# Kernel tuning notes

Hardware: AMD Instinct MI355X
Metric: run time of the kernel (lower is better)

The kernel has to match this reference:

```python
import jax, jax.numpy as jnp
import numpy as np

BATCH, IN_DIM, OUT_DIM = 4096, 8192, 16384

# Each of the 16 logic gates is affine in {1, a, b, a*b}. Rows below give the
# coefficients (const, a, b, ab) for gate k, matching the torch `gate` match-case.
_GATE_COEFS = np.array([
    [0, 0, 0, 0],    # 0: zeros
    [0, 0, 0, 1],    # 1: a*b
    [0, 1, 0, -1],   # 2: a - a*b
    [0, 1, 0, 0],    # 3: a
    [0, 0, 1, -1],   # 4: b - a*b
    [0, 0, 1, 0],    # 5: b
    [0, 1, 1, -2],   # 6: a + b - 2ab (xor)
    [0, 1, 1, -1],   # 7: a + b - ab (or)
    [1, -1, -1, 1],  # 8: 1 - (a + b - ab) (nor)
    [1, -1, -1, 2],  # 9: 1 - (a + b - 2ab) (xnor)
    [1, 0, -1, 0],   # 10: 1 - b
    [1, 0, -1, 1],   # 11: 1 - b + ab
    [1, -1, 0, 0],   # 12: 1 - a
    [1, -1, 0, 1],   # 13: 1 - a + ab
    [1, 0, 0, -1],   # 14: 1 - ab (nand)
    [1, 0, 0, 0],    # 15: ones
], dtype=np.float32)


def setup_inputs() -> dict:
    key = jax.random.key(0)
    k1, k2, k3, k4 = jax.random.split(key, 4)
    x = jax.random.uniform(k1, (BATCH, IN_DIM), dtype=jnp.float32)
    weights = jax.random.normal(k2, (OUT_DIM, 16), dtype=jnp.float32)
    idx_a = jax.random.randint(k3, (OUT_DIM,), 0, IN_DIM, dtype=jnp.int32)
    idx_b = jax.random.randint(k4, (OUT_DIM,), 0, IN_DIM, dtype=jnp.int32)
    return {"x": x, "weights": weights, "idx_a": idx_a, "idx_b": idx_b}


def reference(x, weights, idx_a, idx_b):
    # Training path: softmax over the 16 gate logits per output neuron.
    w = jax.nn.softmax(weights, axis=-1)            # [O, 16]
    # Collapse the 16-gate weighted sum into 4 affine coefficients per neuron.
    coef = w @ jnp.asarray(_GATE_COEFS)             # [O, 4] -> (c0, ca, cb, cab)
    a = x[..., idx_a]                               # [B, O] gather
    b = x[..., idx_b]                               # [B, O] gather
    return coef[:, 0] + coef[:, 1] * a + coef[:, 2] * b + coef[:, 3] * (a * b)
```

## Files before the change

kernel.cpp:

```cpp
#include <hip/hip_runtime.h>
#include <cstddef>
#include <cstdint>

constexpr int BATCH   = 4096;
constexpr int IN_DIM  = 8192;
constexpr int OUT_DIM = 16384;
constexpr int THREADS = 512;
constexpr int RPB     = 4;
constexpr int NBLK    = BATCH / RPB;
constexpr int OPT     = 4;
constexpr int CHUNKS  = OUT_DIM / (THREADS * OPT);
constexpr int SSTEPS  = (IN_DIM / 4) / THREADS;

typedef float    f32x4 __attribute__((ext_vector_type(4)));
typedef uint32_t u32x2 __attribute__((ext_vector_type(2)));

__device__ __forceinline__ uint32_t f2bf(float f) {
  uint32_t u = __float_as_uint(f);
  u += 0x7fffu + ((u >> 16) & 1u);
  return u >> 16;
}
__device__ __forceinline__ uint32_t pack_bf(float a, float b) {
  return f2bf(a) | (f2bf(b) << 16);
}
__device__ __forceinline__ float bf_lo(uint32_t u) { return __uint_as_float(u << 16); }
__device__ __forceinline__ float bf_hi(uint32_t u) { return __uint_as_float(u & 0xffff0000u); }

__global__ __launch_bounds__(64)
void coef_kernel(const float* __restrict__ weights,
                 const int* __restrict__ idx_a,
                 const int* __restrict__ idx_b,
                 float4* __restrict__ coef,
                 uint32_t* __restrict__ pidx) {
  const int o = blockIdx.x * 64 + threadIdx.x;
  if (o >= OUT_DIM) return;

  const float4* wp = reinterpret_cast<const float4*>(weights + (size_t)o * 16);
  float4 t0 = wp[0], t1 = wp[1], t2 = wp[2], t3 = wp[3];
  float w[16] = { t0.x, t0.y, t0.z, t0.w, t1.x, t1.y, t1.z, t1.w,
                  t2.x, t2.y, t2.z, t2.w, t3.x, t3.y, t3.z, t3.w };
  float m = w[0];
#pragma unroll
  for (int i = 1; i < 16; ++i) m = fmaxf(m, w[i]);
  float p[16]; float s = 0.f;
#pragma unroll
  for (int i = 0; i < 16; ++i) { p[i] = __expf(w[i] - m); s += p[i]; }
  const float inv = 1.0f / s;
  const float GC[16]  = {0,0,0,0, 0,0,0,0, 1,1,1,1, 1,1,1,1};
  const float GA[16]  = {0,0,1,1, 0,0,1,1, -1,-1,0,0, -1,-1,0,0};
  const float GB[16]  = {0,0,0,0, 1,1,1,1, -1,-1,-1,-1, 0,0,0,0};
  const float GAB[16] = {0,1,-1,0, -1,0,-2,-1, 1,2,0,1, 0,1,-1,0};
  float c0 = 0.f, ca = 0.f, cb = 0.f, cab = 0.f;
#pragma unroll
  for (int i = 0; i < 16; ++i) {
    c0 += p[i] * GC[i]; ca += p[i] * GA[i];
    cb += p[i] * GB[i]; cab += p[i] * GAB[i];
  }
  coef[o] = make_float4(c0 * inv, ca * inv, cb * inv, cab * inv);
  pidx[o] = (uint32_t)idx_a[o] | ((uint32_t)idx_b[o] << 16);
}

__device__ __forceinline__ float2 eval2(float4 c, uint32_t ga, uint32_t gb) {
  const float a0 = bf_lo(ga), b0 = bf_lo(gb);
  const float a1 = bf_hi(ga), b1 = bf_hi(gb);
  float2 r;
  r.x = fmaf(fmaf(c.w, a0, c.z), b0, fmaf(c.y, a0, c.x));
  r.y = fmaf(fmaf(c.w, a1, c.z), b1, fmaf(c.y, a1, c.x));
  return r;
}

__global__ __launch_bounds__(THREADS)
void logic_main(const float* __restrict__ x,
                const float4* __restrict__ coef,
                const uint32_t* __restrict__ pidx,
                float* __restrict__ out) {
  __shared__ u32x2 xq[IN_DIM];

  const int t  = threadIdx.x;
  const int b0 = blockIdx.x * RPB;

  const f32x4* __restrict__ r0 =
      reinterpret_cast<const f32x4*>(x + (size_t)(b0 + 0) * IN_DIM);
  const f32x4* __restrict__ r1 =
      reinterpret_cast<const f32x4*>(x + (size_t)(b0 + 1) * IN_DIM);
  const f32x4* __restrict__ r2 =
      reinterpret_cast<const f32x4*>(x + (size_t)(b0 + 2) * IN_DIM);
  const f32x4* __restrict__ r3 =
      reinterpret_cast<const f32x4*>(x + (size_t)(b0 + 3) * IN_DIM);

  int o0 = t * OPT;
  int4   pi = *reinterpret_cast<const int4*>(pidx + o0);
  float4 c0 = coef[o0 + 0], c1 = coef[o0 + 1],
         c2 = coef[o0 + 2], c3 = coef[o0 + 3];

#pragma unroll
  for (int s = 0; s < SSTEPS; ++s) {
    const int q = s * THREADS + t;
    f32x4 a = r0[q], b = r1[q], c = r2[q], d = r3[q];
    u32x2 p0, p1, p2, p3;
    p0.x = pack_bf(a.x, b.x); p0.y = pack_bf(c.x, d.x);
    p1.x = pack_bf(a.y, b.y); p1.y = pack_bf(c.y, d.y);
    p2.x = pack_bf(a.z, b.z); p2.y = pack_bf(c.z, d.z);
    p3.x = pack_bf(a.w, b.w); p3.y = pack_bf(c.w, d.w);
    xq[4 * q + 0] = p0;
    xq[4 * q + 1] = p1;
    xq[4 * q + 2] = p2;
    xq[4 * q + 3] = p3;
  }
  __syncthreads();

#pragma unroll 2
  for (int ch = 0; ch < CHUNKS; ++ch) {
    const int o = ch * (THREADS * OPT) + t * OPT;

    const uint32_t i0a = (uint32_t)pi.x & 0xffffu, i0b = (uint32_t)pi.x >> 16;
    const uint32_t i1a = (uint32_t)pi.y & 0xffffu, i1b = (uint32_t)pi.y >> 16;
    const uint32_t i2a = (uint32_t)pi.z & 0xffffu, i2b = (uint32_t)pi.z >> 16;
    const uint32_t i3a = (uint32_t)pi.w & 0xffffu, i3b = (uint32_t)pi.w >> 16;

    const u32x2 g0a = xq[i0a], g0b = xq[i0b];
    const u32x2 g1a = xq[i1a], g1b = xq[i1b];
    const u32x2 g2a = xq[i2a], g2b = xq[i2b];
    const u32x2 g3a = xq[i3a], g3b = xq[i3b];

    const float2 e0lo = eval2(c0, g0a.x, g0b.x), e0hi = eval2(c0, g0a.y, g0b.y);
    const float2 e1lo = eval2(c1, g1a.x, g1b.x), e1hi = eval2(c1, g1a.y, g1b.y);
    const float2 e2lo = eval2(c2, g2a.x, g2b.x), e2hi = eval2(c2, g2a.y, g2b.y);
    const float2 e3lo = eval2(c3, g3a.x, g3b.x), e3hi = eval2(c3, g3a.y, g3b.y);

    f32x4 res0, res1, res2, res3;
    res0.x = e0lo.x; res0.y = e1lo.x; res0.z = e2lo.x; res0.w = e3lo.x;
    res1.x = e0lo.y; res1.y = e1lo.y; res1.z = e2lo.y; res1.w = e3lo.y;
    res2.x = e0hi.x; res2.y = e1hi.x; res2.z = e2hi.x; res2.w = e3hi.x;
    res3.x = e0hi.y; res3.y = e1hi.y; res3.z = e2hi.y; res3.w = e3hi.y;

    if (ch + 1 < CHUNKS) {
      const int on = o + THREADS * OPT;
      pi = *reinterpret_cast<const int4*>(pidx + on);
      c0 = coef[on + 0]; c1 = coef[on + 1];
      c2 = coef[on + 2]; c3 = coef[on + 3];
    }

    *reinterpret_cast<f32x4*>(out + (size_t)(b0 + 0) * OUT_DIM + o) = res0;
    *reinterpret_cast<f32x4*>(out + (size_t)(b0 + 1) * OUT_DIM + o) = res1;
    *reinterpret_cast<f32x4*>(out + (size_t)(b0 + 2) * OUT_DIM + o) = res2;
    *reinterpret_cast<f32x4*>(out + (size_t)(b0 + 3) * OUT_DIM + o) = res3;
  }
}

extern "C" void kernel_launch(void* const* d_in, const int* in_sizes, int n_in,
                              void* d_out, int out_size, void* d_ws, size_t ws_size,
                              hipStream_t stream) {
  const float* x       = (const float*)d_in[0];
  const float* weights = (const float*)d_in[1];
  const int*   idx_a   = (const int*)d_in[2];
  const int*   idx_b   = (const int*)d_in[3];
  float*       out     = (float*)d_out;

  float4*   coef = (float4*)d_ws;
  uint32_t* pidx = (uint32_t*)((char*)d_ws + (size_t)OUT_DIM * 16);

  coef_kernel<<<OUT_DIM / 64, 64, 0, stream>>>(weights, idx_a, idx_b, coef, pidx);
  logic_main<<<NBLK, THREADS, 0, stream>>>(x, coef, pidx, out);
}
```

Before: 97.61 us.

## Double-buffer x rows in LDS and prefetch next row pair during compute

Each block now handles 8 batch rows as four pairs, with two 32 KB LDS buffers holding bf16-packed row pairs. The next pair's global loads are issued into registers before the current pair's gather/compute loop, then packed into the alternate buffer, so global load latency overlaps with LDS gather work. This halves the grid, reloads coef/pidx once per pair, and adds register pressure from the 8 prefetched vectors per thread. It also sets a minimum-blocks-per-CU launch bound.

```diff
diff --git a/kernel.cpp b/kernel.cpp
--- a/kernel.cpp
+++ b/kernel.cpp
@@ -6,14 +6,15 @@
 constexpr int IN_DIM  = 8192;
 constexpr int OUT_DIM = 16384;
 constexpr int THREADS = 512;
-constexpr int RPB     = 4;
-constexpr int NBLK    = BATCH / RPB;
+constexpr int ROWS    = 8;
+constexpr int PAIRS   = ROWS / 2;
+constexpr int NBLK    = BATCH / ROWS;
 constexpr int OPT     = 4;
 constexpr int CHUNKS  = OUT_DIM / (THREADS * OPT);
 constexpr int SSTEPS  = (IN_DIM / 4) / THREADS;
 
 typedef float    f32x4 __attribute__((ext_vector_type(4)));
-typedef uint32_t u32x2 __attribute__((ext_vector_type(2)));
+typedef uint32_t u32x4 __attribute__((ext_vector_type(4)));
 
 __device__ __forceinline__ uint32_t f2bf(float f) {
   uint32_t u = __float_as_uint(f);
@@ -69,82 +70,113 @@
   return r;
 }
 
-__global__ __launch_bounds__(THREADS)
+__global__ __launch_bounds__(THREADS, 4)
 void logic_main(const float* __restrict__ x,
                 const float4* __restrict__ coef,
                 const uint32_t* __restrict__ pidx,
                 float* __restrict__ out) {
-  __shared__ u32x2 xq[IN_DIM];
+  __shared__ uint32_t seg0[IN_DIM];
+  __shared__ uint32_t seg1[IN_DIM];
 
-  const int t  = threadIdx.x;
-  const int b0 = blockIdx.x * RPB;
+  const int t    = threadIdx.x;
+  const int row0 = blockIdx.x * ROWS;
 
-  const f32x4* __restrict__ r0 =
-      reinterpret_cast<const f32x4*>(x + (size_t)(b0 + 0) * IN_DIM);
-  const f32x4* __restrict__ r1 =
-      reinterpret_cast<const f32x4*>(x + (size_t)(b0 + 1) * IN_DIM);
-  const f32x4* __restrict__ r2 =
-      reinterpret_cast<const f32x4*>(x + (size_t)(b0 + 2) * IN_DIM);
-  const f32x4* __restrict__ r3 =
-      reinterpret_cast<const f32x4*>(x + (size_t)(b0 + 3) * IN_DIM);
+  f32x4 la[SSTEPS], lb[SSTEPS];
 
-  int o0 = t * OPT;
-  int4   pi = *reinterpret_cast<const int4*>(pidx + o0);
-  float4 c0 = coef[o0 + 0], c1 = coef[o0 + 1],
-         c2 = coef[o0 + 2], c3 = coef[o0 + 3];
-
+  {
+    const f32x4* __restrict__ rA =
+        reinterpret_cast<const f32x4*>(x + (size_t)row0 * IN_DIM);
+    const f32x4* __restrict__ rB =
+        reinterpret_cast<const f32x4*>(x + (size_t)(row0 + 1) * IN_DIM);
 #pragma unroll
-  for (int s = 0; s < SSTEPS; ++s) {
-    const int q = s * THREADS + t;
-    f32x4 a = r0[q], b = r1[q], c = r2[q], d = r3[q];
-    u32x2 p0, p1, p2, p3;
-    p0.x = pack_bf(a.x, b.x); p0.y = pack_bf(c.x, d.x);
-    p1.x = pack_bf(a.y, b.y); p1.y = pack_bf(c.y, d.y);
-    p2.x = pack_bf(a.z, b.z); p2.y = pack_bf(c.z, d.z);
-    p3.x = pack_bf(a.w, b.w); p3.y = pack_bf(c.w, d.w);
-    xq[4 * q + 0] = p0;
-    xq[4 * q + 1] = p1;
-    xq[4 * q + 2] = p2;
-    xq[4 * q + 3] = p3;
+    for (int s = 0; s < SSTEPS; ++s) {
+      const int q = s * THREADS + t;
+      la[s] = rA[q]; lb[s] = rB[q];
+    }
+#pragma unroll
+    for (int s = 0; s < SSTEPS; ++s) {
+      const int q = s * THREADS + t;
+      u32x4 pk;
+      pk.x = pack_bf(la[s].x, lb[s].x);
+      pk.y = pack_bf(la[s].y, lb[s].y);
+      pk.z = pack_bf(la[s].z, lb[s].z);
+      pk.w = pack_bf(la[s].w, lb[s].w);
+      *reinterpret_cast<u32x4*>(&seg0[4 * q]) = pk;
+    }
   }
   __syncthreads();
 
-#pragma unroll 2
-  for (int ch = 0; ch < CHUNKS; ++ch) {
-    const int o = ch * (THREADS * OPT) + t * OPT;
+  for (int p = 0; p < PAIRS; ++p) {
+    const int bLo = row0 + 2 * p;
+    const uint32_t* __restrict__ seg = (p & 1) ? seg1 : seg0;
+    uint32_t* __restrict__ nxt = (p & 1) ? seg0 : seg1;
 
-    const uint32_t i0a = (uint32_t)pi.x & 0xffffu, i0b = (uint32_t)pi.x >> 16;
-    const uint32_t i1a = (uint32_t)pi.y & 0xffffu, i1b = (uint32_t)pi.y >> 16;
-    const uint32_t i2a = (uint32_t)pi.z & 0xffffu, i2b = (uint32_t)pi.z >> 16;
-    const uint32_t i3a = (uint32_t)pi.w & 0xffffu, i3b = (uint32_t)pi.w >> 16;
-
-    const u32x2 g0a = xq[i0a], g0b = xq[i0b];
-    const u32x2 g1a = xq[i1a], g1b = xq[i1b];
-    const u32x2 g2a = xq[i2a], g2b = xq[i2b];
-    const u32x2 g3a = xq[i3a], g3b = xq[i3b];
-
-    const float2 e0lo = eval2(c0, g0a.x, g0b.x), e0hi = eval2(c0, g0a.y, g0b.y);
-    const float2 e1lo = eval2(c1, g1a.x, g1b.x), e1hi = eval2(c1, g1a.y, g1b.y);
-    const float2 e2lo = eval2(c2, g2a.x, g2b.x), e2hi = eval2(c2, g2a.y, g2b.y);
-    const float2 e3lo = eval2(c3, g3a.x, g3b.x), e3hi = eval2(c3, g3a.y, g3b.y);
-
-    f32x4 res0, res1, res2, res3;
-    res0.x = e0lo.x; res0.y = e1lo.x; res0.z = e2lo.x; res0.w = e3lo.x;
-    res1.x = e0lo.y; res1.y = e1lo.y; res1.z = e2lo.y; res1.w = e3lo.y;
-    res2.x = e0hi.x; res2.y = e1hi.x; res2.z = e2hi.x; res2.w = e3hi.x;
-    res3.x = e0hi.y; res3.y = e1hi.y; res3.z = e2hi.y; res3.w = e3hi.y;
-
-    if (ch + 1 < CHUNKS) {
-      const int on = o + THREADS * OPT;
-      pi = *reinterpret_cast<const int4*>(pidx + on);
-      c0 = coef[on + 0]; c1 = coef[on + 1];
-      c2 = coef[on + 2]; c3 = coef[on + 3];
+    if (p + 1 < PAIRS) {
+      const f32x4* __restrict__ rA =
+          reinterpret_cast<const f32x4*>(x + (size_t)(bLo + 2) * IN_DIM);
+      const f32x4* __restrict__ rB =
+          reinterpret_cast<const f32x4*>(x + (size_t)(bLo + 3) * IN_DIM);
+#pragma unroll
+      for (int s = 0; s < SSTEPS; ++s) {
+        const int q = s * THREADS + t;
+        la[s] = rA[q]; lb[s] = rB[q];
+      }
     }
 
-    *reinterpret_cast<f32x4*>(out + (size_t)(b0 + 0) * OUT_DIM + o) = res0;
-    *reinterpret_cast<f32x4*>(out + (size_t)(b0 + 1) * OUT_DIM + o) = res1;
-    *reinterpret_cast<f32x4*>(out + (size_t)(b0 + 2) * OUT_DIM + o) = res2;
-    *reinterpret_cast<f32x4*>(out + (size_t)(b0 + 3) * OUT_DIM + o) = res3;
+    {
+      int o0 = t * OPT;
+      int4   pi = *reinterpret_cast<const int4*>(pidx + o0);
+      float4 c0 = coef[o0 + 0], c1 = coef[o0 + 1],
+             c2 = coef[o0 + 2], c3 = coef[o0 + 3];
+
+#pragma unroll 2
+      for (int ch = 0; ch < CHUNKS; ++ch) {
+        const int o = ch * (THREADS * OPT) + t * OPT;
+
+        const uint32_t i0a = (uint32_t)pi.x & 0xffffu, i0b = (uint32_t)pi.x >> 16;
+        const uint32_t i1a = (uint32_t)pi.y & 0xffffu, i1b = (uint32_t)pi.y >> 16;
+        const uint32_t i2a = (uint32_t)pi.z & 0xffffu, i2b = (uint32_t)pi.z >> 16;
+        const uint32_t i3a = (uint32_t)pi.w & 0xffffu, i3b = (uint32_t)pi.w >> 16;
+
+        const uint32_t g0a = seg[i0a], g0b = seg[i0b];
+        const uint32_t g1a = seg[i1a], g1b = seg[i1b];
+        const uint32_t g2a = seg[i2a], g2b = seg[i2b];
+        const uint32_t g3a = seg[i3a], g3b = seg[i3b];
+
+        const float2 e0 = eval2(c0, g0a, g0b);
+        const float2 e1 = eval2(c1, g1a, g1b);
+        const float2 e2 = eval2(c2, g2a, g2b);
+        const float2 e3 = eval2(c3, g3a, g3b);
+
+        f32x4 resLo, resHi;
+        resLo.x = e0.x; resLo.y = e1.x; resLo.z = e2.x; resLo.w = e3.x;
+        resHi.x = e0.y; resHi.y = e1.y; resHi.z = e2.y; resHi.w = e3.y;
+
+        if (ch + 1 < CHUNKS) {
+          const int on = o + THREADS * OPT;
+          pi = *reinterpret_cast<const int4*>(pidx + on);
+          c0 = coef[on + 0]; c1 = coef[on + 1];
+          c2 = coef[on + 2]; c3 = coef[on + 3];
+        }
+
+        *reinterpret_cast<f32x4*>(out + (size_t)(bLo + 0) * OUT_DIM + o) = resLo;
+        *reinterpret_cast<f32x4*>(out + (size_t)(bLo + 1) * OUT_DIM + o) = resHi;
+      }
+    }
+
+    if (p + 1 < PAIRS) {
+#pragma unroll
+      for (int s = 0; s < SSTEPS; ++s) {
+        const int q = s * THREADS + t;
+        u32x4 pk;
+        pk.x = pack_bf(la[s].x, lb[s].x);
+        pk.y = pack_bf(la[s].y, lb[s].y);
+        pk.z = pack_bf(la[s].z, lb[s].z);
+        pk.w = pack_bf(la[s].w, lb[s].w);
+        *reinterpret_cast<u32x4*>(&nxt[4 * q]) = pk;
+      }
+      __syncthreads();
+    }
   }
 }
 
```

Result: slower. 102.4 us (+4.9%).

## Stage fp32 input rows into LDS via direct global-to-LDS DMA, two rows per block

Applied to the files above, without the earlier changes.

Replaces the register-staged bf16 packing of four batch rows with `global_load_lds` DMA of two fp32 rows straight into shared memory, and halves rows per block. This removes the VGPR round-trip and the bf16 convert/pack ALU work, and restores full fp32 input precision. In exchange, each gathered output value now needs separate scalar LDS reads per row instead of one packed 8-byte read covering four rows, so LDS gather traffic per output roughly doubles. The block count also doubles, which adds more rereads of the coefficient and index data.

```diff
diff --git a/kernel.cpp b/kernel.cpp
--- a/kernel.cpp
+++ b/kernel.cpp
@@ -6,25 +6,18 @@
 constexpr int IN_DIM  = 8192;
 constexpr int OUT_DIM = 16384;
 constexpr int THREADS = 512;
-constexpr int RPB     = 4;
+constexpr int RPB     = 2;
 constexpr int NBLK    = BATCH / RPB;
 constexpr int OPT     = 4;
 constexpr int CHUNKS  = OUT_DIM / (THREADS * OPT);
-constexpr int SSTEPS  = (IN_DIM / 4) / THREADS;
 
-typedef float    f32x4 __attribute__((ext_vector_type(4)));
-typedef uint32_t u32x2 __attribute__((ext_vector_type(2)));
+typedef float f32x4 __attribute__((ext_vector_type(4)));
 
-__device__ __forceinline__ uint32_t f2bf(float f) {
-  uint32_t u = __float_as_uint(f);
-  u += 0x7fffu + ((u >> 16) & 1u);
-  return u >> 16;
+__device__ __forceinline__ void dma16(const float* g, float* l) {
+  __builtin_amdgcn_global_load_lds(
+      (const __attribute__((address_space(1))) uint32_t*)g,
+      (__attribute__((address_space(3))) uint32_t*)l, 16, 0, 0);
 }
-__device__ __forceinline__ uint32_t pack_bf(float a, float b) {
-  return f2bf(a) | (f2bf(b) << 16);
-}
-__device__ __forceinline__ float bf_lo(uint32_t u) { return __uint_as_float(u << 16); }
-__device__ __forceinline__ float bf_hi(uint32_t u) { return __uint_as_float(u & 0xffff0000u); }
 
 __global__ __launch_bounds__(64)
 void coef_kernel(const float* __restrict__ weights,
@@ -60,53 +53,35 @@
   pidx[o] = (uint32_t)idx_a[o] | ((uint32_t)idx_b[o] << 16);
 }
 
-__device__ __forceinline__ float2 eval2(float4 c, uint32_t ga, uint32_t gb) {
-  const float a0 = bf_lo(ga), b0 = bf_lo(gb);
-  const float a1 = bf_hi(ga), b1 = bf_hi(gb);
-  float2 r;
-  r.x = fmaf(fmaf(c.w, a0, c.z), b0, fmaf(c.y, a0, c.x));
-  r.y = fmaf(fmaf(c.w, a1, c.z), b1, fmaf(c.y, a1, c.x));
-  return r;
-}
-
 __global__ __launch_bounds__(THREADS)
 void logic_main(const float* __restrict__ x,
                 const float4* __restrict__ coef,
                 const uint32_t* __restrict__ pidx,
                 float* __restrict__ out) {
-  __shared__ u32x2 xq[IN_DIM];
+  __shared__ float rowA[IN_DIM];
+  __shared__ float rowB[IN_DIM];
 
-  const int t  = threadIdx.x;
-  const int b0 = blockIdx.x * RPB;
+  const int t    = threadIdx.x;
+  const int lane = t & 63;
+  const int wv   = t >> 6;
+  const int b0   = blockIdx.x * RPB;
 
-  const f32x4* __restrict__ r0 =
-      reinterpret_cast<const f32x4*>(x + (size_t)(b0 + 0) * IN_DIM);
-  const f32x4* __restrict__ r1 =
-      reinterpret_cast<const f32x4*>(x + (size_t)(b0 + 1) * IN_DIM);
-  const f32x4* __restrict__ r2 =
-      reinterpret_cast<const f32x4*>(x + (size_t)(b0 + 2) * IN_DIM);
-  const f32x4* __restrict__ r3 =
-      reinterpret_cast<const f32x4*>(x + (size_t)(b0 + 3) * IN_DIM);
+  {
+    const float* __restrict__ src0 = x + (size_t)b0 * IN_DIM;
+    const float* __restrict__ src1 = x + (size_t)(b0 + 1) * IN_DIM;
+#pragma unroll
+    for (int s = 0; s < 4; ++s) {
+      const int off = (wv * 4 + s) * 256 + lane * 4;
+      dma16(src0 + off, rowA + off);
+      dma16(src1 + off, rowB + off);
+    }
+  }
 
   int o0 = t * OPT;
   int4   pi = *reinterpret_cast<const int4*>(pidx + o0);
   float4 c0 = coef[o0 + 0], c1 = coef[o0 + 1],
          c2 = coef[o0 + 2], c3 = coef[o0 + 3];
 
-#pragma unroll
-  for (int s = 0; s < SSTEPS; ++s) {
-    const int q = s * THREADS + t;
-    f32x4 a = r0[q], b = r1[q], c = r2[q], d = r3[q];
-    u32x2 p0, p1, p2, p3;
-    p0.x = pack_bf(a.x, b.x); p0.y = pack_bf(c.x, d.x);
-    p1.x = pack_bf(a.y, b.y); p1.y = pack_bf(c.y, d.y);
-    p2.x = pack_bf(a.z, b.z); p2.y = pack_bf(c.z, d.z);
-    p3.x = pack_bf(a.w, b.w); p3.y = pack_bf(c.w, d.w);
-    xq[4 * q + 0] = p0;
-    xq[4 * q + 1] = p1;
-    xq[4 * q + 2] = p2;
-    xq[4 * q + 3] = p3;
-  }
   __syncthreads();
 
 #pragma unroll 2
@@ -118,21 +93,20 @@
     const uint32_t i2a = (uint32_t)pi.z & 0xffffu, i2b = (uint32_t)pi.z >> 16;
     const uint32_t i3a = (uint32_t)pi.w & 0xffffu, i3b = (uint32_t)pi.w >> 16;
 
-    const u32x2 g0a = xq[i0a], g0b = xq[i0b];
-    const u32x2 g1a = xq[i1a], g1b = xq[i1b];
-    const u32x2 g2a = xq[i2a], g2b = xq[i2b];
-    const u32x2 g3a = xq[i3a], g3b = xq[i3b];
+    const float a0A = rowA[i0a], b0A = rowA[i0b], a0B = rowB[i0a], b0B = rowB[i0b];
+    const float a1A = rowA[i1a], b1A = rowA[i1b], a1B = rowB[i1a], b1B = rowB[i1b];
+    const float a2A = rowA[i2a], b2A = rowA[i2b], a2B = rowB[i2a], b2B = rowB[i2b];
+    const float a3A = rowA[i3a], b3A = rowA[i3b], a3B = rowB[i3a], b3B = rowB[i3b];
 
-    const float2 e0lo = eval2(c0, g0a.x, g0b.x), e0hi = eval2(c0, g0a.y, g0b.y);
-    const float2 e1lo = eval2(c1, g1a.x, g1b.x), e1hi = eval2(c1, g1a.y, g1b.y);
-    const float2 e2lo = eval2(c2, g2a.x, g2b.x), e2hi = eval2(c2, g2a.y, g2b.y);
-    const float2 e3lo = eval2(c3, g3a.x, g3b.x), e3hi = eval2(c3, g3a.y, g3b.y);
-
-    f32x4 res0, res1, res2, res3;
-    res0.x = e0lo.x; res0.y = e1lo.x; res0.z = e2lo.x; res0.w = e3lo.x;
-    res1.x = e0lo.y; res1.y = e1lo.y; res1.z = e2lo.y; res1.w = e3lo.y;
-    res2.x = e0hi.x; res2.y = e1hi.x; res2.z = e2hi.x; res2.w = e3hi.x;
-    res3.x = e0hi.y; res3.y = e1hi.y; res3.z = e2hi.y; res3.w = e3hi.y;
+    f32x4 resA, resB;
+    resA.x = fmaf(fmaf(c0.w, a0A, c0.z), b0A, fmaf(c0.y, a0A, c0.x));
+    resB.x = fmaf(fmaf(c0.w, a0B, c0.z), b0B, fmaf(c0.y, a0B, c0.x));
+    resA.y = fmaf(fmaf(c1.w, a1A, c1.z), b1A, fmaf(c1.y, a1A, c1.x));
+    resB.y = fmaf(fmaf(c1.w, a1B, c1.z), b1B, fmaf(c1.y, a1B, c1.x));
+    resA.z = fmaf(fmaf(c2.w, a2A, c2.z), b2A, fmaf(c2.y, a2A, c2.x));
+    resB.z = fmaf(fmaf(c2.w, a2B, c2.z), b2B, fmaf(c2.y, a2B, c2.x));
+    resA.w = fmaf(fmaf(c3.w, a3A, c3.z), b3A, fmaf(c3.y, a3A, c3.x));
+    resB.w = fmaf(fmaf(c3.w, a3B, c3.z), b3B, fmaf(c3.y, a3B, c3.x));
 
     if (ch + 1 < CHUNKS) {
       const int on = o + THREADS * OPT;
@@ -141,10 +115,8 @@
       c2 = coef[on + 2]; c3 = coef[on + 3];
     }
 
-    *reinterpret_cast<f32x4*>(out + (size_t)(b0 + 0) * OUT_DIM + o) = res0;
-    *reinterpret_cast<f32x4*>(out + (size_t)(b0 + 1) * OUT_DIM + o) = res1;
-    *reinterpret_cast<f32x4*>(out + (size_t)(b0 + 2) * OUT_DIM + o) = res2;
-    *reinterpret_cast<f32x4*>(out + (size_t)(b0 + 3) * OUT_DIM + o) = res3;
+    *reinterpret_cast<f32x4*>(out + (size_t)(b0 + 0) * OUT_DIM + o) = resA;
+    *reinterpret_cast<f32x4*>(out + (size_t)(b0 + 1) * OUT_DIM + o) = resB;
   }
 }
 
```

Measured after the change: 111.6 us. 1.14x slower.
